# Kernel optimization log

Hardware: AMD Instinct MI355X
Metric: run time of the kernel (lower is better)

The kernel has to match this reference:

```python
import jax, jax.numpy as jnp
import numpy as np

N = 12288
NUM_GRAPHS = 64


def setup_inputs() -> dict:
    key = jax.random.key(0)
    k1, k2, k3 = jax.random.split(key, 3)
    scores = jax.random.normal(k1, (N,), dtype=jnp.float32)
    labels = jax.random.randint(k2, (N,), 0, 2, dtype=jnp.int32)
    segment_ids = jnp.sort(jax.random.randint(k3, (N,), 0, NUM_GRAPHS, dtype=jnp.int32))
    return {"scores": scores, "labels": labels, "segment_ids": segment_ids}


def reference(scores, labels, segment_ids):
    # Pair (i, j) is valid iff: same graph, label[i] == 1 (pos), label[j] == 0 (neg).
    lab = labels.astype(jnp.bool_)
    same_graph = segment_ids[:, None] == segment_ids[None, :]          # [N, N]
    mask = same_graph & lab[:, None] & (~lab)[None, :]                 # [N, N]
    diff = scores[:, None] - scores[None, :]                           # s_pos - s_neg
    hinge = jnp.maximum(1.0 - diff, 0.0)
    total = jnp.sum(jnp.where(mask, hinge, 0.0))
    cnt = jnp.sum(mask).astype(scores.dtype)
    # mean over all pairs; zero loss (== mean(scores*0)) if no pairs exist
    loss = jnp.where(cnt > 0, total / jnp.maximum(cnt, 1.0), jnp.zeros((), scores.dtype))
    return loss
```

## Files before the change

kernel.cpp:

```cpp
#include <hip/hip_runtime.h>


#define NUM_GRAPHS 64
#define BLOCK 256
#define CAP 4096

__global__ __launch_bounds__(BLOCK)
void pairwise_fused(const float* __restrict__ scores,
                    const int* __restrict__ labels,
                    const int* __restrict__ seg,
                    int n,
                    float* __restrict__ g_tot,
                    unsigned long long* __restrict__ g_cnt,
                    unsigned int* __restrict__ g_done,
                    float* __restrict__ out) {
    __shared__ float s_pos[CAP];
    __shared__ float s_neg[CAP];
    __shared__ int s_cp, s_cn, s_loA, s_loB, s_start, s_end;
    __shared__ float sm[BLOCK / 64];
    __shared__ unsigned long long smc[BLOCK / 64];

    const int g    = blockIdx.x;
    const int tid  = threadIdx.x;
    const int lane = tid & 63;
    const int wave = tid >> 6;
    const unsigned long long below = (1ull << lane) - 1ull;

    if (tid == 0) { s_cp = 0; s_cn = 0; s_loA = -1; s_loB = -1; s_start = 0; s_end = 0; }
    __syncthreads();

    const int stride = (n + BLOCK - 1) / BLOCK;
    if (stride <= 64) {
        int pos = tid * stride;
        int v = (pos < n) ? seg[pos] : 0x7fffffff;
        unsigned long long mA = __ballot(v < g);
        unsigned long long mB = __ballot(v < g + 1);
        if (mA && lane == 63 - __clzll(mA)) atomicMax(&s_loA, pos);
        if (mB && lane == 63 - __clzll(mB)) atomicMax(&s_loB, pos);
        __syncthreads();

        if (wave == 0) {
            int L = s_loA;
            int idx = L + 1 + lane;
            bool pred = (lane < stride) && (idx < n) && (seg[idx] < g);
            unsigned long long m = __ballot(pred);
            if (lane == 0) s_start = L + 1 + __popcll(m);
        } else if (wave == 1) {
            int L = s_loB;
            int idx = L + 1 + lane;
            bool pred = (lane < stride) && (idx < n) && (seg[idx] < g + 1);
            unsigned long long m = __ballot(pred);
            if (lane == 0) s_end = L + 1 + __popcll(m);
        }
    } else {
        if (tid == 0) {
            int lo = 0, hi = n;
            while (lo < hi) { int m = (lo + hi) >> 1; if (seg[m] < g) lo = m + 1; else hi = m; }
            s_start = lo;
            lo = 0; hi = n;
            while (lo < hi) { int m = (lo + hi) >> 1; if (seg[m] < g + 1) lo = m + 1; else hi = m; }
            s_end = lo;
        }
    }
    __syncthreads();
    const int start = s_start, end = s_end;

    for (int bi = start + wave * 64; bi < end; bi += BLOCK) {
        int i = bi + lane;
        bool valid = i < end;
        int   lab = valid ? labels[i] : 0;
        float sc  = valid ? scores[i] : 0.0f;
        bool isp = valid && (lab != 0);
        bool isn = valid && (lab == 0);
        unsigned long long pm = __ballot(isp);
        unsigned long long nm = __ballot(isn);
        int pb = 0, nb = 0;
        if (lane == 0) {
            pb = atomicAdd(&s_cp, __popcll(pm));
            nb = atomicAdd(&s_cn, __popcll(nm));
        }
        pb = __shfl(pb, 0, 64);
        nb = __shfl(nb, 0, 64);
        if (isp) { int r = pb + __popcll(pm & below); if (r < CAP) s_pos[r] = sc; }
        else if (isn) { int r = nb + __popcll(nm & below); if (r < CAP) s_neg[r] = sc; }
    }
    __syncthreads();

    const int np = s_cp, nn = s_cn;
    float local = 0.0f;
    unsigned long long pairs = 0ull;

    if (np <= CAP && nn <= CAP) {
        for (int p = tid; p < np; p += BLOCK) {
            const float base = 1.0f - s_pos[p];
            int j = 0;
            for (; j + 4 <= nn; j += 4) {
                local += fmaxf(base + s_neg[j],     0.0f);
                local += fmaxf(base + s_neg[j + 1], 0.0f);
                local += fmaxf(base + s_neg[j + 2], 0.0f);
                local += fmaxf(base + s_neg[j + 3], 0.0f);
            }
            for (; j < nn; ++j) local += fmaxf(base + s_neg[j], 0.0f);
        }
        if (tid == 0) pairs = (unsigned long long)np * (unsigned long long)nn;
    } else {
        for (int i = start + tid; i < end; i += BLOCK) {
            if (labels[i] != 0) {
                const float base = 1.0f - scores[i];
                for (int j = start; j < end; ++j) {
                    if (labels[j] == 0) { local += fmaxf(base + scores[j], 0.0f); pairs++; }
                }
            }
        }
    }

    for (int off = 32; off; off >>= 1) {
        local += __shfl_down(local, off, 64);
        pairs += __shfl_down(pairs, off, 64);
    }
    if (lane == 0) { sm[wave] = local; smc[wave] = pairs; }
    __syncthreads();

    if (tid == 0) {
        float tot = 0.0f;
        unsigned long long c = 0ull;
        #pragma unroll
        for (int w = 0; w < BLOCK / 64; ++w) { tot += sm[w]; c += smc[w]; }
        atomicAdd(g_tot, tot);
        atomicAdd(g_cnt, c);
        __threadfence();
        unsigned int ticket = atomicAdd(g_done, 1u);
        if (ticket == gridDim.x - 1) {
            float T = atomicAdd(g_tot, 0.0f);
            unsigned long long C = atomicAdd(g_cnt, 0ull);
            out[0] = (C > 0) ? (T / (float)C) : 0.0f;
        }
    }
}

extern "C" void kernel_launch(void* const* d_in, const int* in_sizes, int n_in,
                              void* d_out, int out_size, void* d_ws, size_t ws_size,
                              hipStream_t stream) {
    const float* scores = (const float*)d_in[0];
    const int*   labels = (const int*)d_in[1];
    const int*   seg    = (const int*)d_in[2];
    float*       out    = (float*)d_out;
    const int n = in_sizes[0];

    float*              g_tot  = (float*)d_ws;
    unsigned long long* g_cnt  = (unsigned long long*)((char*)d_ws + 8);
    unsigned int*       g_done = (unsigned int*)((char*)d_ws + 16);

    hipMemsetAsync(d_ws, 0, 24, stream);
    pairwise_fused<<<NUM_GRAPHS, BLOCK, 0, stream>>>(scores, labels, seg, n,
                                                     g_tot, g_cnt, g_done, out);
}
```

Baseline: 66.76 us.

## Prefetch per-graph window into LDS and replace atomic finalize with second kernel

Each block now speculatively loads a window of scores and labels around its expected segment range into shared memory before the segment-boundary search. This overlaps those global loads with the search and removes the dependent global reads in the partition loop; if the real range falls outside the window it falls back to global memory. The memset, global atomics and last-block ticket are replaced by per-graph partial outputs plus a tiny 64-thread finalize kernel, which costs an extra launch. The pos/neg shared buffers shrink from 4096 to 1024 entries.

After: 61.85 us. 7.4% less time.

```diff
diff --git a/kernel.cpp b/kernel.cpp
--- a/kernel.cpp
+++ b/kernel.cpp
@@ -3,17 +3,19 @@
 
 #define NUM_GRAPHS 64
 #define BLOCK 256
-#define CAP 4096
+#define SLACK 384
+#define WCAP 1024
+#define CAP 1024
 
 __global__ __launch_bounds__(BLOCK)
-void pairwise_fused(const float* __restrict__ scores,
-                    const int* __restrict__ labels,
-                    const int* __restrict__ seg,
-                    int n,
-                    float* __restrict__ g_tot,
-                    unsigned long long* __restrict__ g_cnt,
-                    unsigned int* __restrict__ g_done,
-                    float* __restrict__ out) {
+void pairwise_per_graph(const float* __restrict__ scores,
+                        const int* __restrict__ labels,
+                        const int* __restrict__ seg,
+                        int n,
+                        float* __restrict__ tots,
+                        long long* __restrict__ cnts) {
+    __shared__ float s_wsc[WCAP];
+    __shared__ int   s_wlb[WCAP];
     __shared__ float s_pos[CAP];
     __shared__ float s_neg[CAP];
     __shared__ int s_cp, s_cn, s_loA, s_loB, s_start, s_end;
@@ -27,9 +29,20 @@
     const unsigned long long below = (1ull << lane) - 1ull;
 
     if (tid == 0) { s_cp = 0; s_cn = 0; s_loA = -1; s_loB = -1; s_start = 0; s_end = 0; }
-    __syncthreads();
+
+    const int avg = n / NUM_GRAPHS;
+    int wlo = g * avg - SLACK;       if (wlo < 0) wlo = 0;
+    int whi = (g + 1) * avg + SLACK; if (whi > n) whi = n;
+    const int wlen = whi - wlo;
+    if (wlen <= WCAP) {
+        for (int k = tid; k < wlen; k += BLOCK) {
+            s_wsc[k] = scores[wlo + k];
+            s_wlb[k] = labels[wlo + k];
+        }
+    }
 
     const int stride = (n + BLOCK - 1) / BLOCK;
+    __syncthreads();
     if (stride <= 64) {
         int pos = tid * stride;
         int v = (pos < n) ? seg[pos] : 0x7fffffff;
@@ -38,7 +51,6 @@
         if (mA && lane == 63 - __clzll(mA)) atomicMax(&s_loA, pos);
         if (mB && lane == 63 - __clzll(mB)) atomicMax(&s_loB, pos);
         __syncthreads();
-
         if (wave == 0) {
             int L = s_loA;
             int idx = L + 1 + lane;
@@ -64,12 +76,17 @@
     }
     __syncthreads();
     const int start = s_start, end = s_end;
+    const bool windowed = (wlen <= WCAP) && (start >= wlo) && (end <= whi);
 
     for (int bi = start + wave * 64; bi < end; bi += BLOCK) {
         int i = bi + lane;
         bool valid = i < end;
-        int   lab = valid ? labels[i] : 0;
-        float sc  = valid ? scores[i] : 0.0f;
+        int   lab = 0;
+        float sc  = 0.0f;
+        if (valid) {
+            if (windowed) { lab = s_wlb[i - wlo]; sc = s_wsc[i - wlo]; }
+            else          { lab = labels[i];      sc = scores[i];      }
+        }
         bool isp = valid && (lab != 0);
         bool isn = valid && (lab == 0);
         unsigned long long pm = __ballot(isp);
@@ -81,7 +98,7 @@
         }
         pb = __shfl(pb, 0, 64);
         nb = __shfl(nb, 0, 64);
-        if (isp) { int r = pb + __popcll(pm & below); if (r < CAP) s_pos[r] = sc; }
+        if (isp)      { int r = pb + __popcll(pm & below); if (r < CAP) s_pos[r] = sc; }
         else if (isn) { int r = nb + __popcll(nm & below); if (r < CAP) s_neg[r] = sc; }
     }
     __syncthreads();
@@ -126,16 +143,23 @@
         unsigned long long c = 0ull;
         #pragma unroll
         for (int w = 0; w < BLOCK / 64; ++w) { tot += sm[w]; c += smc[w]; }
-        atomicAdd(g_tot, tot);
-        atomicAdd(g_cnt, c);
-        __threadfence();
-        unsigned int ticket = atomicAdd(g_done, 1u);
-        if (ticket == gridDim.x - 1) {
-            float T = atomicAdd(g_tot, 0.0f);
-            unsigned long long C = atomicAdd(g_cnt, 0ull);
-            out[0] = (C > 0) ? (T / (float)C) : 0.0f;
-        }
+        tots[g] = tot;
+        cnts[g] = (long long)c;
     }
+}
+
+__global__ __launch_bounds__(64)
+void pairwise_finalize(const long long* __restrict__ cnts,
+                       const float* __restrict__ tots,
+                       float* __restrict__ out) {
+    const int t = threadIdx.x;
+    float tot = tots[t];
+    long long c = cnts[t];
+    for (int off = 32; off; off >>= 1) {
+        tot += __shfl_down(tot, off, 64);
+        c   += __shfl_down(c,   off, 64);
+    }
+    if (t == 0) out[0] = (c > 0) ? (tot / (float)c) : 0.0f;
 }
 
 extern "C" void kernel_launch(void* const* d_in, const int* in_sizes, int n_in,
@@ -147,11 +171,9 @@
     float*       out    = (float*)d_out;
     const int n = in_sizes[0];
 
-    float*              g_tot  = (float*)d_ws;
-    unsigned long long* g_cnt  = (unsigned long long*)((char*)d_ws + 8);
-    unsigned int*       g_done = (unsigned int*)((char*)d_ws + 16);
+    long long* cnts = (long long*)d_ws;
+    float*     tots = (float*)((char*)d_ws + NUM_GRAPHS * sizeof(long long));
 
-    hipMemsetAsync(d_ws, 0, 24, stream);
-    pairwise_fused<<<NUM_GRAPHS, BLOCK, 0, stream>>>(scores, labels, seg, n,
-                                                     g_tot, g_cnt, g_done, out);
+    pairwise_per_graph<<<NUM_GRAPHS, BLOCK, 0, stream>>>(scores, labels, seg, n, tots, cnts);
+    pairwise_finalize<<<1, 64, 0, stream>>>(cnts, tots, out);
 }
```
